# Kernel optimization log

Hardware: AMD Instinct MI355X
Metric: run time of the kernel (lower is better)

The kernel has to match this reference:

```python
import jax, jax.numpy as jnp
import numpy as np

B, S, D = 2, 2048, 1024
N, M, HD = 16, 4, 64          # query heads, kv heads, head dim
G = N // M                    # GQA group size
V = 32000
GIN = 12                      # gate input dim
ROPE_THETA = 1024.0
ROT = int(HD * 0.5)           # partial rotary dim = 32
EPS = 1e-6
STD = 0.006


def setup_inputs() -> dict:
    key = jax.random.key(0)
    ks = jax.random.split(key, 10)
    tn = lambda k, shape: (STD * jax.random.truncated_normal(k, -3, 3, shape)).astype(jnp.float32)
    return {
        "x": jax.random.normal(ks[0], (B, S, D), jnp.float32),
        "token_ids": jax.random.randint(ks[1], (B, S), 0, V),
        "mask": jnp.tril(jnp.ones((S, S), dtype=bool)),  # causal
        "w_q": tn(ks[2], (D, N * HD)),
        "w_k": tn(ks[3], (D, M * HD)),
        "w_v": tn(ks[4], (D, M * HD)),
        "w_o": tn(ks[5], (N * HD, D)),  # zeros at init; random for a meaningful baseline
        "ve_embed": tn(ks[6], (V, M * HD)),
        "value_lambda": jnp.full((), 0.5, jnp.float32),
        "ve_lambda": jnp.full((), 0.5, jnp.float32),
        "ve_gate": tn(ks[7], (GIN, M)),
        "attn_gate": tn(ks[8], (GIN, N)),
    }


def _qk_norm(t):
    var = jnp.mean(jnp.square(t.astype(jnp.float32)), axis=-1, keepdims=True)
    return (t * jax.lax.rsqrt(var + EPS)).astype(t.dtype)


def _rope(t):
    # partial rotary: rotate first ROT dims only
    half = ROT // 2
    inv_freq = 1.0 / ROPE_THETA ** (jnp.arange(half, dtype=jnp.float32) / half)
    ang = jnp.arange(S, dtype=jnp.float32)[:, None] * inv_freq[None, :]
    cos = jnp.cos(ang)[None, :, None, :]  # [1,S,1,half]
    sin = jnp.sin(ang)[None, :, None, :]
    rot, pas = t[..., :ROT], t[..., ROT:]
    x1, x2 = jnp.split(rot, 2, axis=-1)
    return jnp.concatenate([x1 * cos - x2 * sin, x2 * cos + x1 * sin, pas], axis=-1)


def reference(x, token_ids, mask, w_q, w_k, w_v, w_o, ve_embed,
              value_lambda, ve_lambda, ve_gate, attn_gate):
    q = (x @ w_q).reshape(B, S, N, HD)
    k = (x @ w_k).reshape(B, S, M, HD)
    v = (x @ w_v).reshape(B, S, M, HD)
    q = _rope(_qk_norm(q))
    k = _rope(_qk_norm(k))

    # value-embedding lambda mixing with sigmoid gate
    ve = ve_embed[token_ids].reshape(B, S, M, HD)
    ve_g = 2.0 * jax.nn.sigmoid(x[..., :GIN] @ ve_gate)       # [B,S,M]
    v = value_lambda * v + ve_lambda * ve_g[..., None] * ve

    # GQA causal attention (group q heads over kv heads, no kv repeat)
    qg = q.reshape(B, S, M, G, HD)
    scale = 1.0 / np.sqrt(HD).astype(np.float32)
    scores = jnp.einsum('bqmgd,bkmd->bmgqk', qg, k) * scale   # [B,M,G,S,S]
    scores = jnp.where(mask[None, None, None], scores, jnp.float32(-1e30))
    p = jax.nn.softmax(scores, axis=-1)
    attn = jnp.einsum('bmgqk,bkmd->bqmgd', p, v).reshape(B, S, N, HD)

    # output sigmoid gate then out-projection
    a_g = 2.0 * jax.nn.sigmoid(x[..., :GIN] @ attn_gate)      # [B,S,N]
    attn = a_g[..., None] * attn
    return attn.reshape(B, S, N * HD) @ w_o
```

## Files before the change

kernel.cpp:

```cpp
#include <hip/hip_runtime.h>
#include <math.h>

#define S_LEN 2048
#define NHEADS 16
#define KVH 4

typedef __attribute__((ext_vector_type(8))) _Float16 half8;
typedef __attribute__((ext_vector_type(4))) _Float16 half4;
typedef __attribute__((ext_vector_type(4))) float f32x4;

__device__ inline void gld16(const void* g, void* l) {
  __builtin_amdgcn_global_load_lds(
      (const __attribute__((address_space(1))) unsigned int*)g,
      (__attribute__((address_space(3))) unsigned int*)l, 16, 0, 0);
}

__global__ __launch_bounds__(256) void xcast(
    const float* __restrict__ x, _Float16* __restrict__ xh)
{
  const size_t i = ((size_t)blockIdx.x * 256 + threadIdx.x) * 8;
  float4 f0 = *(const float4*)(x + i);
  float4 f1 = *(const float4*)(x + i + 4);
  half8 h;
  h[0] = (_Float16)f0.x; h[1] = (_Float16)f0.y; h[2] = (_Float16)f0.z; h[3] = (_Float16)f0.w;
  h[4] = (_Float16)f1.x; h[5] = (_Float16)f1.y; h[6] = (_Float16)f1.z; h[7] = (_Float16)f1.w;
  *(half8*)(xh + i) = h;
}

__global__ __launch_bounds__(256) void setup_fused(
    const float* __restrict__ wq, const float* __restrict__ wk,
    const float* __restrict__ wv, const float* __restrict__ wo,
    const float* __restrict__ x, const float* __restrict__ attn_gate,
    _Float16* __restrict__ wqkvT, _Float16* __restrict__ woT,
    float2* __restrict__ costab, float* __restrict__ ag)
{
  const int t = threadIdx.x;
  int L = blockIdx.x;

  if (L >= 768) {
    const int row = (L - 768) * 16 + (t >> 4);
    const int n = t & 15;
    float z = 0.f;
    #pragma unroll
    for (int i = 0; i < 12; ++i) z += x[(size_t)row * 1024 + i] * attn_gate[i * NHEADS + n];
    ag[(size_t)row * NHEADS + n] = 2.f / (1.f + __expf(-z));
    return;
  }
  if (L >= 640) {
    const int gi = (L - 640) * 256 + t;
    const int s = gi >> 4, i = gi & 15;
    const float ang = (float)s * exp2f(-0.625f * (float)i);
    float c, sn;
    sincosf(ang, &sn, &c);
    costab[gi] = make_float2(c, sn);
    return;
  }

  const float* in; _Float16* out; int C, ct, rt;
  if (L < 256)      { in = wq; out = wqkvT;                       C = 1024; ct = (L & 15) * 64; rt = (L >> 4) * 64; }
  else if (L < 320) { L -= 256; in = wk; out = wqkvT + (size_t)1024 * 1024; C = 256; ct = (L & 3) * 64; rt = (L >> 2) * 64; }
  else if (L < 384) { L -= 320; in = wv; out = wqkvT + (size_t)1280 * 1024; C = 256; ct = (L & 3) * 64; rt = (L >> 2) * 64; }
  else              { L -= 384; in = wo; out = woT;               C = 1024; ct = (L & 15) * 64; rt = (L >> 4) * 64; }

  __shared__ float Ls[64][65];
  {
    const int r = t >> 2, cs = (t & 3) << 4;
    const float* src = in + (size_t)(rt + r) * C + ct + cs;
    #pragma unroll
    for (int j = 0; j < 16; j += 4) {
      float4 v = *(const float4*)(src + j);
      Ls[r][cs + j] = v.x; Ls[r][cs + j + 1] = v.y;
      Ls[r][cs + j + 2] = v.z; Ls[r][cs + j + 3] = v.w;
    }
  }
  __syncthreads();
  {
    const int c = t >> 2, rs = (t & 3) << 4;
    half8 h0, h1;
    #pragma unroll
    for (int j = 0; j < 8; j++) h0[j] = (_Float16)Ls[rs + j][c];
    #pragma unroll
    for (int j = 0; j < 8; j++) h1[j] = (_Float16)Ls[rs + 8 + j][c];
    _Float16* dst = out + (size_t)(ct + c) * 1024 + rt + rs;
    *(half8*)dst = h0;
    *(half8*)(dst + 8) = h1;
  }
}

template<typename OUT_T, bool EPI>
__global__ __launch_bounds__(256) void gemm_k(
    const _Float16* __restrict__ A, const _Float16* __restrict__ BT,
    OUT_T* __restrict__ C, int M, int N, int K, int lda,
    const float2* __restrict__ costab)
{
  __shared__ _Float16 lds[16384];
  const int t = threadIdx.x;
  const int w = t >> 6, l = t & 63;
  const int lg = l >> 4, ll = l & 15;
  const int bm = blockIdx.y * 128, bn = blockIdx.x * 128;
  const int wr = (w >> 1) * 64, wc = (w & 1) * 64;
  const int srow = t >> 2, sslot = t & 3;

  f32x4 acc[4][4] = {};

  auto stage = [&](int k0, int buf) {
    char* Ab = (char*)lds + buf * 8192;
    char* Bb = (char*)lds + 16384 + buf * 8192;
    const int so = (sslot ^ (srow & 3)) << 3;
    gld16(A  + (size_t)(bm + srow)      * lda + k0 + so, Ab + w * 1024);
    gld16(A  + (size_t)(bm + srow + 64) * lda + k0 + so, Ab + 4096 + w * 1024);
    gld16(BT + (size_t)(bn + srow)      * K   + k0 + so, Bb + w * 1024);
    gld16(BT + (size_t)(bn + srow + 64) * K   + k0 + so, Bb + 4096 + w * 1024);
  };

  stage(0, 0);
  __syncthreads();

  int buf = 0;
  for (int k0 = 0; k0 < K; k0 += 32) {
    if (k0 + 32 < K) stage(k0 + 32, buf ^ 1);

    const char* Ab = (const char*)lds + buf * 8192;
    const char* Bb = (const char*)lds + 16384 + buf * 8192;
    half8 af[4], bfr[4];
    #pragma unroll
    for (int mt = 0; mt < 4; mt++) {
      const int row = wr + mt * 16 + ll;
      af[mt] = *(const half8*)(Ab + row * 64 + ((lg ^ (row & 3)) << 4));
    }
    #pragma unroll
    for (int nt = 0; nt < 4; nt++) {
      const int row = wc + nt * 16 + ll;
      bfr[nt] = *(const half8*)(Bb + row * 64 + ((lg ^ (row & 3)) << 4));
    }
    __builtin_amdgcn_s_setprio(1);
    #pragma unroll
    for (int mt = 0; mt < 4; mt++)
      #pragma unroll
      for (int nt = 0; nt < 4; nt++)
        acc[mt][nt] = __builtin_amdgcn_mfma_f32_16x16x32_f16(af[mt], bfr[nt], acc[mt][nt], 0, 0, 0);
    __builtin_amdgcn_s_setprio(0);

    __syncthreads();
    buf ^= 1;
  }

  if constexpr (EPI) {
    const int col0 = bn + wc;
    const int head = col0 >> 6;
    const bool isv = head >= 20;
    const float qs = (head < 16) ? 0.18033688f : 1.0f;
    #pragma unroll
    for (int mt = 0; mt < 4; mt++) {
      if (isv) {
        #pragma unroll
        for (int r = 0; r < 4; r++) {
          const size_t row = (size_t)bm + wr + mt * 16 + lg * 4 + r;
          #pragma unroll
          for (int nt = 0; nt < 4; nt++)
            C[row * N + col0 + nt * 16 + ll] = (OUT_T)acc[mt][nt][r];
        }
      } else {
        float ss[4];
        #pragma unroll
        for (int r = 0; r < 4; r++)
          ss[r] = acc[mt][0][r] * acc[mt][0][r] + acc[mt][1][r] * acc[mt][1][r]
                + acc[mt][2][r] * acc[mt][2][r] + acc[mt][3][r] * acc[mt][3][r];
        #pragma unroll
        for (int mi = 0; mi < 4; mi++) {
          const int msk = 1 << mi;
          #pragma unroll
          for (int r = 0; r < 4; r++) ss[r] += __shfl_xor(ss[r], msk);
        }
        #pragma unroll
        for (int r = 0; r < 4; r++) {
          const size_t row = (size_t)bm + wr + mt * 16 + lg * 4 + r;
          const float inv = rsqrtf(ss[r] * (1.0f / 64.0f) + 1e-6f) * qs;
          const float2 cs2 = costab[(row & (S_LEN - 1)) * 16 + ll];
          const float a0 = acc[mt][0][r] * inv, a1 = acc[mt][1][r] * inv;
          C[row * N + col0 +      ll] = (OUT_T)(a0 * cs2.x - a1 * cs2.y);
          C[row * N + col0 + 16 + ll] = (OUT_T)(a1 * cs2.x + a0 * cs2.y);
          C[row * N + col0 + 32 + ll] = (OUT_T)(acc[mt][2][r] * inv);
          C[row * N + col0 + 48 + ll] = (OUT_T)(acc[mt][3][r] * inv);
        }
      }
    }
  } else {
    #pragma unroll
    for (int mt = 0; mt < 4; mt++) {
      #pragma unroll
      for (int r = 0; r < 4; r++) {
        const size_t row = (size_t)bm + wr + mt * 16 + lg * 4 + r;
        #pragma unroll
        for (int nt = 0; nt < 4; nt++) {
          const int col = bn + wc + nt * 16 + ll;
          if constexpr (sizeof(OUT_T) == 2) C[row * N + col] = (OUT_T)(_Float16)acc[mt][nt][r];
          else                              C[row * N + col] = acc[mt][nt][r];
        }
      }
    }
  }
}

__global__ __launch_bounds__(256) void vtrans_mix(
    const _Float16* __restrict__ qkv, const float* __restrict__ x,
    const int* __restrict__ token_ids, const float* __restrict__ ve_embed,
    const float* __restrict__ ve_gate, const float* __restrict__ vlam,
    const float* __restrict__ velam, _Float16* __restrict__ vT)
{
  __shared__ _Float16 Ls[64][72];
  __shared__ float veg[64];
  __shared__ int toks[64];
  const int st = blockIdx.x * 64;
  const int bm = blockIdx.y;
  const int b = bm >> 2, m = bm & 3;
  const int t = threadIdx.x;

  if (t < 64) {
    const size_t row_g = (size_t)b * S_LEN + st + t;
    toks[t] = token_ids[row_g];
    float z = 0.f;
    #pragma unroll
    for (int i = 0; i < 12; ++i) z += x[row_g * 1024 + i] * ve_gate[i * KVH + m];
    veg[t] = velam[0] * 2.f / (1.f + __expf(-z));
  }
  __syncthreads();
  {
    const int sr = t >> 2, ds = (t & 3) << 4;
    const float vl = vlam[0];
    const _Float16* src = qkv + ((size_t)(b * S_LEN + st + sr)) * 1536 + 1280 + m * 64 + ds;
    const float* ves = ve_embed + (size_t)toks[sr] * 256 + m * 64 + ds;
    half8 v0 = *(const half8*)src;
    half8 v1 = *(const half8*)(src + 8);
    const float g = veg[sr];
    #pragma unroll
    for (int q4 = 0; q4 < 4; q4++) {
      float4 ev = *(const float4*)(ves + q4 * 4);
      const int o0 = q4 * 4;
      Ls[sr][ds + o0 + 0] = (_Float16)(vl * (float)((o0 + 0 < 8) ? v0[o0 + 0] : v1[o0 - 8]) + g * ev.x);
      Ls[sr][ds + o0 + 1] = (_Float16)(vl * (float)((o0 + 1 < 8) ? v0[o0 + 1] : v1[o0 - 7]) + g * ev.y);
      Ls[sr][ds + o0 + 2] = (_Float16)(vl * (float)((o0 + 2 < 8) ? v0[o0 + 2] : v1[o0 - 6]) + g * ev.z);
      Ls[sr][ds + o0 + 3] = (_Float16)(vl * (float)((o0 + 3 < 8) ? v0[o0 + 3] : v1[o0 - 5]) + g * ev.w);
    }
  }
  __syncthreads();
  {
    const int dr = t >> 2, ssl = (t & 3) << 4;
    half8 o0, o1;
    #pragma unroll
    for (int j = 0; j < 8; j++) { o0[j] = Ls[ssl + j][dr]; o1[j] = Ls[ssl + 8 + j][dr]; }
    _Float16* dst = vT + ((size_t)bm * 64 + dr) * S_LEN + st + ssl;
    *(half8*)dst = o0;
    *(half8*)(dst + 8) = o1;
  }
}

__global__ __launch_bounds__(256) void attn_mfma(
    _Float16* __restrict__ qkv, const _Float16* __restrict__ vT,
    const float* __restrict__ ag)
{
  const int L = blockIdx.x;
  const int b = L >> 9, idx = L & 511;
  const int n = idx & 15;
  const int j = idx >> 4;
  const int qt = b ? j : 31 - j;
  const int m = n >> 2;

  const int t = threadIdx.x, w = t >> 6, l = t & 63;
  const int lg = l >> 4, ll = l & 15;

  __shared__ _Float16 lds[20480];

  const int qbase = qt * 64 + w * 16;
  const size_t qrow_g = (size_t)(b * S_LEN) + qbase;

  half8 qa[2];
  #pragma unroll
  for (int s = 0; s < 2; s++)
    qa[s] = *(const half8*)(qkv + (qrow_g + ll) * 1536 + n * 64 + s * 32 + lg * 8);

  f32x4 o[4] = {};
  float lrun = 0.f;

  const int srow = l >> 3, sslot = l & 7;

  auto stage = [&](int kt, int buf) {
    #pragma unroll
    for (int i = 0; i < 2; i++) {
      const int kr = w * 16 + i * 8 + srow;
      const size_t kg = ((size_t)(b * S_LEN + kt * 64 + kr)) * 1536 + 1024 + m * 64
                        + ((sslot ^ (kr & 7)) << 3);
      gld16(qkv + kg, (char*)lds + buf * 8192 + w * 2048 + i * 1024);
      const int vr = w * 16 + i * 8 + srow;
      const size_t vg = ((size_t)((b * KVH + m) * 64 + vr)) * S_LEN + kt * 64
                        + ((sslot ^ (vr & 7)) << 3);
      gld16(vT + vg, (char*)lds + 16384 + buf * 8192 + w * 2048 + i * 1024);
    }
  };

  stage(0, 0);
  __syncthreads();

  for (int kt = 0; kt <= qt; kt++) {
    const int cur = kt & 1;
    if (kt < qt) stage(kt + 1, cur ^ 1);

    const char* Ksb = (const char*)lds + cur * 8192;
    const char* Vsb = (const char*)lds + 16384 + cur * 8192;
    char* Psb = (char*)lds + 32768;

    f32x4 sc[4] = {};
    __builtin_amdgcn_s_setprio(1);
    #pragma unroll
    for (int s = 0; s < 2; s++)
      #pragma unroll
      for (int kf = 0; kf < 4; kf++) {
        const int krow = kf * 16 + ll;
        const half8 kb = *(const half8*)(Ksb + krow * 128
                          + (((4 * s + lg) ^ (krow & 7)) << 4));
        sc[kf] = __builtin_amdgcn_mfma_f32_16x16x32_f16(kb, qa[s], sc[kf], 0, 0, 0);
      }
    __builtin_amdgcn_s_setprio(0);

    if (kt == qt) {
      const int qg = qbase + ll;
      #pragma unroll
      for (int kf = 0; kf < 4; kf++)
        #pragma unroll
        for (int r = 0; r < 4; r++)
          if (kt * 64 + kf * 16 + 4 * lg + r > qg) sc[kf][r] = -1e30f;
    }

    const int q_loc = w * 16 + ll;
    #pragma unroll
    for (int kf = 0; kf < 4; kf++) {
      half4 pk;
      #pragma unroll
      for (int r = 0; r < 4; r++) {
        const float e = exp2f(sc[kf][r] - 11.6f);
        lrun += e;
        pk[r] = (_Float16)e;
      }
      const int slot = (2 * kf + (lg >> 1)) ^ (q_loc & 7);
      *(half4*)(Psb + q_loc * 128 + slot * 16 + (lg & 1) * 8) = pk;
    }

    __builtin_amdgcn_s_setprio(1);
    #pragma unroll
    for (int s = 0; s < 2; s++) {
      const half8 pa = *(const half8*)(Psb + q_loc * 128
                        + (((4 * s + lg) ^ (q_loc & 7)) << 4));
      #pragma unroll
      for (int df = 0; df < 4; df++) {
        const int vrow = df * 16 + ll;
        const half8 vb = *(const half8*)(Vsb + vrow * 128
                          + (((4 * s + lg) ^ (vrow & 7)) << 4));
        o[df] = __builtin_amdgcn_mfma_f32_16x16x32_f16(pa, vb, o[df], 0, 0, 0);
      }
    }
    __builtin_amdgcn_s_setprio(0);

    __syncthreads();
  }

  lrun += __shfl_xor(lrun, 16);
  lrun += __shfl_xor(lrun, 32);
  float lr[4];
  #pragma unroll
  for (int r = 0; r < 4; r++) lr[r] = __shfl(lrun, lg * 4 + r);
  #pragma unroll
  for (int r = 0; r < 4; r++) {
    const size_t qrow = qrow_g + lg * 4 + r;
    const float scale = ag[qrow * NHEADS + n] / lr[r];
    #pragma unroll
    for (int df = 0; df < 4; df++)
      qkv[qrow * 1536 + n * 64 + df * 16 + ll] = (_Float16)(o[df][r] * scale);
  }
}

extern "C" void kernel_launch(void* const* d_in, const int* in_sizes, int n_in,
                              void* d_out, int out_size, void* d_ws, size_t ws_size,
                              hipStream_t stream) {
  const float* x         = (const float*)d_in[0];
  const int*   token_ids = (const int*)d_in[1];
  const float* w_q       = (const float*)d_in[3];
  const float* w_k       = (const float*)d_in[4];
  const float* w_v       = (const float*)d_in[5];
  const float* w_o       = (const float*)d_in[6];
  const float* ve_embed  = (const float*)d_in[7];
  const float* vlam      = (const float*)d_in[8];
  const float* velam     = (const float*)d_in[9];
  const float* ve_gate   = (const float*)d_in[10];
  const float* attn_gate = (const float*)d_in[11];
  float* out = (float*)d_out;

  char* p = (char*)d_ws;
  _Float16* wqkvT = (_Float16*)p; p += (size_t)1536 * 1024 * 2;
  _Float16* woT   = (_Float16*)p; p += (size_t)1024 * 1024 * 2;
  _Float16* qkv   = (_Float16*)p; p += (size_t)4096 * 1536 * 2;
  _Float16* vTb   = (_Float16*)p; p += (size_t)8 * 64 * S_LEN * 2;
  float*    ag    = (float*)p;    p += (size_t)4096 * NHEADS * 4;

  _Float16* xh = (_Float16*)d_out;
  float2* costab = (float2*)((char*)d_out + (size_t)12 * 1024 * 1024);

  dim3 blk(256);
  setup_fused<<<dim3(1024), blk, 0, stream>>>(w_q, w_k, w_v, w_o, x, attn_gate,
                                              wqkvT, woT, costab, ag);
  xcast<<<dim3(2048), blk, 0, stream>>>(x, xh);

  gemm_k<_Float16, true><<<dim3(12, 32), blk, 0, stream>>>(
      xh, wqkvT, qkv, 4096, 1536, 1024, 1024, costab);

  vtrans_mix<<<dim3(32, 8), blk, 0, stream>>>(qkv, x, token_ids, ve_embed,
                                              ve_gate, vlam, velam, vTb);

  attn_mfma<<<dim3(1024), blk, 0, stream>>>(qkv, vTb, ag);

  gemm_k<float, false><<<dim3(8, 32), blk, 0, stream>>>(
      qkv, woT, out, 4096, 1024, 1024, 1536, nullptr);
}
```

Measured before the change: 106.7 us.

## Fuse x cast into setup kernel and reorder attention block scheduling

Merges the standalone fp32-to-fp16 cast of x into the setup kernel as extra blocks, each handling 16 elements per thread, which removes one kernel launch. Attention blocks are re-indexed so the longest causal query tiles of both batches are scheduled first, interleaved by batch and head, to improve load balance. The attention gate values are now loaded before the main loop, so their latency overlaps the computation instead of sitting in the epilogue. Costs are slightly more register use and a larger setup grid.

```diff
diff --git a/kernel.cpp b/kernel.cpp
--- a/kernel.cpp
+++ b/kernel.cpp
@@ -13,18 +13,6 @@
   __builtin_amdgcn_global_load_lds(
       (const __attribute__((address_space(1))) unsigned int*)g,
       (__attribute__((address_space(3))) unsigned int*)l, 16, 0, 0);
-}
-
-__global__ __launch_bounds__(256) void xcast(
-    const float* __restrict__ x, _Float16* __restrict__ xh)
-{
-  const size_t i = ((size_t)blockIdx.x * 256 + threadIdx.x) * 8;
-  float4 f0 = *(const float4*)(x + i);
-  float4 f1 = *(const float4*)(x + i + 4);
-  half8 h;
-  h[0] = (_Float16)f0.x; h[1] = (_Float16)f0.y; h[2] = (_Float16)f0.z; h[3] = (_Float16)f0.w;
-  h[4] = (_Float16)f1.x; h[5] = (_Float16)f1.y; h[6] = (_Float16)f1.z; h[7] = (_Float16)f1.w;
-  *(half8*)(xh + i) = h;
 }
 
 __global__ __launch_bounds__(256) void setup_fused(
@@ -32,11 +20,25 @@
     const float* __restrict__ wv, const float* __restrict__ wo,
     const float* __restrict__ x, const float* __restrict__ attn_gate,
     _Float16* __restrict__ wqkvT, _Float16* __restrict__ woT,
-    float2* __restrict__ costab, float* __restrict__ ag)
+    float2* __restrict__ costab, float* __restrict__ ag,
+    _Float16* __restrict__ xh)
 {
   const int t = threadIdx.x;
   int L = blockIdx.x;
 
+  if (L >= 1024) {
+    const size_t i = ((size_t)(L - 1024) * 256 + t) * 16;
+    #pragma unroll
+    for (int c = 0; c < 2; c++) {
+      float4 f0 = *(const float4*)(x + i + c * 8);
+      float4 f1 = *(const float4*)(x + i + c * 8 + 4);
+      half8 h;
+      h[0] = (_Float16)f0.x; h[1] = (_Float16)f0.y; h[2] = (_Float16)f0.z; h[3] = (_Float16)f0.w;
+      h[4] = (_Float16)f1.x; h[5] = (_Float16)f1.y; h[6] = (_Float16)f1.z; h[7] = (_Float16)f1.w;
+      *(half8*)(xh + i + c * 8) = h;
+    }
+    return;
+  }
   if (L >= 768) {
     const int row = (L - 768) * 16 + (t >> 4);
     const int n = t & 15;
@@ -260,10 +262,9 @@
     const float* __restrict__ ag)
 {
   const int L = blockIdx.x;
-  const int b = L >> 9, idx = L & 511;
-  const int n = idx & 15;
-  const int j = idx >> 4;
-  const int qt = b ? j : 31 - j;
+  const int qt = 31 - (L >> 5);
+  const int b = (L >> 4) & 1;
+  const int n = L & 15;
   const int m = n >> 2;
 
   const int t = threadIdx.x, w = t >> 6, l = t & 63;
@@ -278,6 +279,11 @@
   #pragma unroll
   for (int s = 0; s < 2; s++)
     qa[s] = *(const half8*)(qkv + (qrow_g + ll) * 1536 + n * 64 + s * 32 + lg * 8);
+
+  float agr[4];
+  #pragma unroll
+  for (int r = 0; r < 4; r++)
+    agr[r] = ag[(qrow_g + lg * 4 + r) * NHEADS + n];
 
   f32x4 o[4] = {};
   float lrun = 0.f;
@@ -371,7 +377,7 @@
   #pragma unroll
   for (int r = 0; r < 4; r++) {
     const size_t qrow = qrow_g + lg * 4 + r;
-    const float scale = ag[qrow * NHEADS + n] / lr[r];
+    const float scale = agr[r] / lr[r];
     #pragma unroll
     for (int df = 0; df < 4; df++)
       qkv[qrow * 1536 + n * 64 + df * 16 + ll] = (_Float16)(o[df][r] * scale);
@@ -405,9 +411,8 @@
   float2* costab = (float2*)((char*)d_out + (size_t)12 * 1024 * 1024);
 
   dim3 blk(256);
-  setup_fused<<<dim3(1024), blk, 0, stream>>>(w_q, w_k, w_v, w_o, x, attn_gate,
-                                              wqkvT, woT, costab, ag);
-  xcast<<<dim3(2048), blk, 0, stream>>>(x, xh);
+  setup_fused<<<dim3(2048), blk, 0, stream>>>(w_q, w_k, w_v, w_o, x, attn_gate,
+                                              wqkvT, woT, costab, ag, xh);
 
   gemm_k<_Float16, true><<<dim3(12, 32), blk, 0, stream>>>(
       xh, wqkvT, qkv, 4096, 1536, 1024, 1024, costab);
```

Measured after the change: 100.5 us. 1.06x faster.
